# Kernel tuning notes

Measured on AMD Instinct MI355X. Metric: run time of the kernel, lower is better.

Reference implementation:

```python
import jax, jax.numpy as jnp
import numpy as np

E = 2_000_000   # edges
N = 200_000     # atoms
B = 100         # bond types (10 species, ordered pairs)
R = 13          # reduced_matrix_element (SK integrals per bond)
G = 512         # num_xgrid
T = 10          # atom types
OE = 4          # n_onsite_Es
R_MIN, R_MAX = 1.0, 6.0  # SK table distance range (Bohr-ish)


def setup_inputs() -> dict:
    key = jax.random.key(0)
    k1, k2, k3, k4, k5, k6 = jax.random.split(key, 6)
    rij = jax.random.uniform(k1, (E,), jnp.float32, 1.5, 5.5)
    edge_type = jax.random.randint(k2, (E,), 0, B, jnp.int32)
    atom_type = jax.random.randint(k3, (N,), 0, T, jnp.int32)
    xx = jnp.linspace(R_MIN, R_MAX, G, dtype=jnp.float32)  # sorted distance grid
    hopping_param = jax.random.normal(k4, (B, R, G), jnp.float32)
    overlap_param = jax.random.normal(k5, (B, R, G), jnp.float32)
    onsite_param = jax.random.normal(k6, (T, OE, 1), jnp.float32)
    return {"rij": rij, "edge_type": edge_type, "atom_type": atom_type,
            "xx": xx, "hopping_param": hopping_param,
            "overlap_param": overlap_param, "onsite_param": onsite_param}


def _interp_by_type(rij, edge_type, xx, table):
    """Fused gather + linear interpolation, keyed by edge_type.

    Replaces the original per-bond-type masked loop: for each edge, pick the
    [R, G] SK table for its bond type and linearly interpolate along the
    distance grid at rij. Returns [E, R].
    """
    g = xx.shape[0]
    # interval index for each edge (clamped -> linear extrapolation at edges)
    idx = jnp.clip(jnp.searchsorted(xx, rij, side="right") - 1, 0, g - 2)  # [E]
    x0 = xx[idx]
    x1 = xx[idx + 1]
    t = ((rij - x0) / (x1 - x0))[:, None]  # [E, 1]
    # advanced indexing on axes 0 and 2, full slice on axis 1 -> [E, R]
    y0 = table[edge_type, :, idx]
    y1 = table[edge_type, :, idx + 1]
    return y0 * (1.0 - t) + y1 * t


def reference(rij, edge_type, atom_type, xx, hopping_param, overlap_param, onsite_param):
    edge_features = _interp_by_type(rij, edge_type, xx, hopping_param)   # [E, R]
    edge_overlap = _interp_by_type(rij, edge_type, xx, overlap_param)    # [E, R]
    # dftb onsite: direct per-atom-type parameter lookup (num_paras == 1)
    node_features = onsite_param[atom_type, :, 0]                         # [N, OE]
    return edge_features, edge_overlap, node_features
```

## Files before the change

### kernel.cpp

```cpp
#include <hip/hip_runtime.h>

#define E_CNT 2000000
#define N_CNT 200000
#define B_CNT 100
#define R_CNT 13
#define G_CNT 512
#define T_CNT 10
#define OE_CNT 4

#define P_ROW 16
#define P_ONE ((size_t)B_CNT * G_CNT * P_ROW)
#define P_BYTES_TOTAL (2 * P_ONE * 4)

#define EDGES_PER_BLOCK 64
#define EDGE_BLOCKS (E_CNT / EDGES_PER_BLOCK)
#define NODE_BLOCKS ((N_CNT + 255) / 256)
#define OUT_OVL_OFF ((size_t)E_CNT * R_CNT)
#define OUT_NODE_OFF ((size_t)2 * E_CNT * R_CNT)

#define SH_STRIDE 20

__global__ __launch_bounds__(256) void repack2_kernel(
    const float* __restrict__ hopping,
    const float* __restrict__ overlap,
    float* __restrict__ Ph,
    float* __restrict__ Po)
{
    int tid = blockIdx.x * 256 + threadIdx.x;
    int g = tid & (G_CNT - 1);
    int br = tid >> 9;
    int r = br % R_CNT;
    int b = br / R_CNT;
    size_t src = (size_t)tid;
    size_t dst = ((size_t)(b * G_CNT + g)) * P_ROW + r;
    Ph[dst] = hopping[src];
    Po[dst] = overlap[src];
}

template <bool DO_NODES>
__global__ __launch_bounds__(256) void pass_kernel(
    const float* __restrict__ rij,
    const int*   __restrict__ edge_type,
    const float* __restrict__ P,
    const int*   __restrict__ atom_type,
    const float* __restrict__ onsite,
    float* __restrict__ out,
    float* __restrict__ out_nodes)
{
    if (blockIdx.x < EDGE_BLOCKS) {
        __shared__ float sh[EDGES_PER_BLOCK * SH_STRIDE];

        int tid = threadIdx.x;
        int eL = tid >> 2;
        int j  = tid & 3;
        int e  = blockIdx.x * EDGES_PER_BLOCK + eL;

        float r = rij[e];
        int b = edge_type[e];

        const float inv_dx = 511.0f / 5.0f;
        float s = (r - 1.0f) * inv_dx;
        int idx = (int)s;
        idx = max(0, min(G_CNT - 2, idx));
        float t = s - (float)idx;
        float omt = 1.0f - t;

        size_t base = ((size_t)((b << 9) + idx)) * P_ROW + 4 * j;
        float4 y0 = *(const float4*)(P + base);
        float4 y1 = *(const float4*)(P + base + P_ROW);

        float4 v;
        v.x = y0.x * omt + y1.x * t;
        v.y = y0.y * omt + y1.y * t;
        v.z = y0.z * omt + y1.z * t;
        v.w = y0.w * omt + y1.w * t;

        *(float4*)(sh + eL * SH_STRIDE + 4 * j) = v;
        __syncthreads();

        if (tid < 208) {
            unsigned f0 = (unsigned)tid * 4u;
            float4 q;
            float* qs = (float*)&q;
            #pragma unroll
            for (int k = 0; k < 4; ++k) {
                unsigned f = f0 + k;
                unsigned ee = f / 13u;
                unsigned rr = f - ee * 13u;
                qs[k] = sh[ee * SH_STRIDE + rr];
            }
            *(float4*)(out + (size_t)blockIdx.x * (EDGES_PER_BLOCK * R_CNT) + f0) = q;
        }
    } else if (DO_NODES) {
        int n = (blockIdx.x - EDGE_BLOCKS) * 256 + threadIdx.x;
        if (n < N_CNT) {
            int t = atom_type[n];
            float4 v;
            v.x = onsite[t * OE_CNT + 0];
            v.y = onsite[t * OE_CNT + 1];
            v.z = onsite[t * OE_CNT + 2];
            v.w = onsite[t * OE_CNT + 3];
            *(float4*)(out_nodes + (size_t)n * OE_CNT) = v;
        }
    }
}

__global__ __launch_bounds__(256) void dftbsk_fallback(
    const float* __restrict__ rij,
    const int*   __restrict__ edge_type,
    const int*   __restrict__ atom_type,
    const float* __restrict__ xx,
    const float* __restrict__ hopping,
    const float* __restrict__ overlap,
    const float* __restrict__ onsite,
    float*       __restrict__ out)
{
    __shared__ float sxx[G_CNT];
    for (int i = threadIdx.x; i < G_CNT; i += blockDim.x) sxx[i] = xx[i];
    __syncthreads();

    long long gid = (long long)blockIdx.x * blockDim.x + threadIdx.x;
    if (gid < E_CNT) {
        int e = (int)gid;
        float r = rij[e];
        int b = edge_type[e];
        const float inv_dx = (float)(G_CNT - 1) / 5.0f;
        int idx = (int)floorf((r - 1.0f) * inv_dx);
        idx = max(0, min(G_CNT - 2, idx));
        while (idx > 0 && r < sxx[idx]) --idx;
        while (idx < G_CNT - 2 && r >= sxx[idx + 1]) ++idx;
        float x0 = sxx[idx], x1 = sxx[idx + 1];
        float t = (r - x0) / (x1 - x0);
        float omt = 1.0f - t;
        const float* hb = hopping + (size_t)b * (R_CNT * G_CNT) + idx;
        const float* ob = overlap + (size_t)b * (R_CNT * G_CNT) + idx;
        float* outh = out + (size_t)e * R_CNT;
        float* outo = out + OUT_OVL_OFF + (size_t)e * R_CNT;
        #pragma unroll
        for (int rr = 0; rr < R_CNT; ++rr)
            outh[rr] = hb[rr * G_CNT] * omt + hb[rr * G_CNT + 1] * t;
        #pragma unroll
        for (int rr = 0; rr < R_CNT; ++rr)
            outo[rr] = ob[rr * G_CNT] * omt + ob[rr * G_CNT + 1] * t;
    } else if (gid < (long long)E_CNT + N_CNT) {
        int n = (int)(gid - E_CNT);
        int t = atom_type[n];
        float4 v;
        v.x = onsite[t * OE_CNT + 0];
        v.y = onsite[t * OE_CNT + 1];
        v.z = onsite[t * OE_CNT + 2];
        v.w = onsite[t * OE_CNT + 3];
        *(float4*)(out + OUT_NODE_OFF + (size_t)n * OE_CNT) = v;
    }
}

extern "C" void kernel_launch(void* const* d_in, const int* in_sizes, int n_in,
                              void* d_out, int out_size, void* d_ws, size_t ws_size,
                              hipStream_t stream) {
    const float* rij        = (const float*)d_in[0];
    const int*   edge_type  = (const int*)d_in[1];
    const int*   atom_type  = (const int*)d_in[2];
    const float* xx         = (const float*)d_in[3];
    const float* hopping    = (const float*)d_in[4];
    const float* overlap    = (const float*)d_in[5];
    const float* onsite     = (const float*)d_in[6];
    float* out = (float*)d_out;

    if (ws_size >= P_BYTES_TOTAL) {
        float* Ph = (float*)d_ws;
        float* Po = Ph + P_ONE;
        const int repack_total = B_CNT * R_CNT * G_CNT;
        repack2_kernel<<<repack_total / 256, 256, 0, stream>>>(hopping, overlap, Ph, Po);
        pass_kernel<true><<<EDGE_BLOCKS + NODE_BLOCKS, 256, 0, stream>>>(
            rij, edge_type, Ph, atom_type, onsite, out, out + OUT_NODE_OFF);
        pass_kernel<false><<<EDGE_BLOCKS, 256, 0, stream>>>(
            rij, edge_type, Po, atom_type, onsite, out + OUT_OVL_OFF, out + OUT_NODE_OFF);
    } else {
        const long long total = (long long)E_CNT + N_CNT;
        const int grid = (int)((total + 255) / 256);
        dftbsk_fallback<<<grid, 256, 0, stream>>>(rij, edge_type, atom_type, xx,
                                                  hopping, overlap, onsite, out);
    }
}
```

Before: 279.0 us.

## Fuse hopping and overlap passes with interleaved table layout and nontemporal IO

Repacks the hopping and overlap tables into one interleaved 128-byte row per (bond type, grid point), so that a single fused kernel interpolates both outputs from adjacent cache lines. This removes the second pass, which re-read rij and edge_type and launched a second large grid. Output and input streams also switch to nontemporal loads and stores, to keep them from displacing the gathered table in cache. In exchange the table footprint doubles per row and each block uses twice the shared memory.

```diff
diff --git a/kernel.cpp b/kernel.cpp
--- a/kernel.cpp
+++ b/kernel.cpp
@@ -8,9 +8,9 @@
 #define T_CNT 10
 #define OE_CNT 4
 
-#define P_ROW 16
-#define P_ONE ((size_t)B_CNT * G_CNT * P_ROW)
-#define P_BYTES_TOTAL (2 * P_ONE * 4)
+#define P2_ROW 32
+#define P2_FLOATS ((size_t)B_CNT * G_CNT * P2_ROW)
+#define P2_BYTES (P2_FLOATS * 4)
 
 #define EDGES_PER_BLOCK 64
 #define EDGE_BLOCKS (E_CNT / EDGES_PER_BLOCK)
@@ -20,43 +20,54 @@
 
 #define SH_STRIDE 20
 
-__global__ __launch_bounds__(256) void repack2_kernel(
+typedef float v4f __attribute__((ext_vector_type(4)));
+
+__global__ __launch_bounds__(256) void repack_interleave_kernel(
     const float* __restrict__ hopping,
     const float* __restrict__ overlap,
-    float* __restrict__ Ph,
-    float* __restrict__ Po)
+    float* __restrict__ P2)
 {
     int tid = blockIdx.x * 256 + threadIdx.x;
+    int b = tid >> 9;
     int g = tid & (G_CNT - 1);
-    int br = tid >> 9;
-    int r = br % R_CNT;
-    int b = br / R_CNT;
-    size_t src = (size_t)tid;
-    size_t dst = ((size_t)(b * G_CNT + g)) * P_ROW + r;
-    Ph[dst] = hopping[src];
-    Po[dst] = overlap[src];
+    float h[16], o[16];
+    #pragma unroll
+    for (int r = 0; r < R_CNT; ++r) {
+        size_t src = (((size_t)b * R_CNT + r) << 9) + g;
+        h[r] = hopping[src];
+        o[r] = overlap[src];
+    }
+    h[13] = h[14] = h[15] = 0.0f;
+    o[13] = o[14] = o[15] = 0.0f;
+    float* dst = P2 + (size_t)tid * P2_ROW;
+    #pragma unroll
+    for (int q = 0; q < 4; ++q) {
+        v4f hv = { h[4*q], h[4*q+1], h[4*q+2], h[4*q+3] };
+        v4f ov = { o[4*q], o[4*q+1], o[4*q+2], o[4*q+3] };
+        *(v4f*)(dst + 4 * q)      = hv;
+        *(v4f*)(dst + 16 + 4 * q) = ov;
+    }
 }
 
-template <bool DO_NODES>
-__global__ __launch_bounds__(256) void pass_kernel(
+__global__ __launch_bounds__(256) void fused_kernel(
     const float* __restrict__ rij,
     const int*   __restrict__ edge_type,
-    const float* __restrict__ P,
+    const float* __restrict__ P2,
     const int*   __restrict__ atom_type,
     const float* __restrict__ onsite,
-    float* __restrict__ out,
-    float* __restrict__ out_nodes)
+    float* __restrict__ out)
 {
     if (blockIdx.x < EDGE_BLOCKS) {
-        __shared__ float sh[EDGES_PER_BLOCK * SH_STRIDE];
+        __shared__ float shh[EDGES_PER_BLOCK * SH_STRIDE];
+        __shared__ float sho[EDGES_PER_BLOCK * SH_STRIDE];
 
         int tid = threadIdx.x;
         int eL = tid >> 2;
         int j  = tid & 3;
         int e  = blockIdx.x * EDGES_PER_BLOCK + eL;
 
-        float r = rij[e];
-        int b = edge_type[e];
+        float r = __builtin_nontemporal_load(rij + e);
+        int   b = __builtin_nontemporal_load(edge_type + e);
 
         const float inv_dx = 511.0f / 5.0f;
         float s = (r - 1.0f) * inv_dx;
@@ -65,42 +76,45 @@
         float t = s - (float)idx;
         float omt = 1.0f - t;
 
-        size_t base = ((size_t)((b << 9) + idx)) * P_ROW + 4 * j;
-        float4 y0 = *(const float4*)(P + base);
-        float4 y1 = *(const float4*)(P + base + P_ROW);
+        const float* row = P2 + ((size_t)((b << 9) + idx)) * P2_ROW + 4 * j;
+        v4f h0 = *(const v4f*)(row);
+        v4f h1 = *(const v4f*)(row + P2_ROW);
+        v4f o0 = *(const v4f*)(row + 16);
+        v4f o1 = *(const v4f*)(row + 16 + P2_ROW);
 
-        float4 v;
-        v.x = y0.x * omt + y1.x * t;
-        v.y = y0.y * omt + y1.y * t;
-        v.z = y0.z * omt + y1.z * t;
-        v.w = y0.w * omt + y1.w * t;
+        v4f vh = h0 * omt + h1 * t;
+        v4f vo = o0 * omt + o1 * t;
 
-        *(float4*)(sh + eL * SH_STRIDE + 4 * j) = v;
+        *(v4f*)(shh + eL * SH_STRIDE + 4 * j) = vh;
+        *(v4f*)(sho + eL * SH_STRIDE + 4 * j) = vo;
         __syncthreads();
 
         if (tid < 208) {
             unsigned f0 = (unsigned)tid * 4u;
-            float4 q;
-            float* qs = (float*)&q;
+            float ph[4], po[4];
             #pragma unroll
             for (int k = 0; k < 4; ++k) {
                 unsigned f = f0 + k;
                 unsigned ee = f / 13u;
                 unsigned rr = f - ee * 13u;
-                qs[k] = sh[ee * SH_STRIDE + rr];
+                ph[k] = shh[ee * SH_STRIDE + rr];
+                po[k] = sho[ee * SH_STRIDE + rr];
             }
-            *(float4*)(out + (size_t)blockIdx.x * (EDGES_PER_BLOCK * R_CNT) + f0) = q;
+            v4f qh = { ph[0], ph[1], ph[2], ph[3] };
+            v4f qo = { po[0], po[1], po[2], po[3] };
+            size_t ob = (size_t)blockIdx.x * (EDGES_PER_BLOCK * R_CNT) + f0;
+            __builtin_nontemporal_store(qh, (v4f*)(out + ob));
+            __builtin_nontemporal_store(qo, (v4f*)(out + OUT_OVL_OFF + ob));
         }
-    } else if (DO_NODES) {
+    } else {
         int n = (blockIdx.x - EDGE_BLOCKS) * 256 + threadIdx.x;
         if (n < N_CNT) {
             int t = atom_type[n];
-            float4 v;
-            v.x = onsite[t * OE_CNT + 0];
-            v.y = onsite[t * OE_CNT + 1];
-            v.z = onsite[t * OE_CNT + 2];
-            v.w = onsite[t * OE_CNT + 3];
-            *(float4*)(out_nodes + (size_t)n * OE_CNT) = v;
+            v4f v = { onsite[t * OE_CNT + 0],
+                      onsite[t * OE_CNT + 1],
+                      onsite[t * OE_CNT + 2],
+                      onsite[t * OE_CNT + 3] };
+            __builtin_nontemporal_store(v, (v4f*)(out + OUT_NODE_OFF + (size_t)n * OE_CNT));
         }
     }
 }
@@ -166,15 +180,12 @@
     const float* onsite     = (const float*)d_in[6];
     float* out = (float*)d_out;
 
-    if (ws_size >= P_BYTES_TOTAL) {
-        float* Ph = (float*)d_ws;
-        float* Po = Ph + P_ONE;
-        const int repack_total = B_CNT * R_CNT * G_CNT;
-        repack2_kernel<<<repack_total / 256, 256, 0, stream>>>(hopping, overlap, Ph, Po);
-        pass_kernel<true><<<EDGE_BLOCKS + NODE_BLOCKS, 256, 0, stream>>>(
-            rij, edge_type, Ph, atom_type, onsite, out, out + OUT_NODE_OFF);
-        pass_kernel<false><<<EDGE_BLOCKS, 256, 0, stream>>>(
-            rij, edge_type, Po, atom_type, onsite, out + OUT_OVL_OFF, out + OUT_NODE_OFF);
+    if (ws_size >= P2_BYTES) {
+        float* P2 = (float*)d_ws;
+        repack_interleave_kernel<<<(B_CNT * G_CNT) / 256, 256, 0, stream>>>(
+            hopping, overlap, P2);
+        fused_kernel<<<EDGE_BLOCKS + NODE_BLOCKS, 256, 0, stream>>>(
+            rij, edge_type, P2, atom_type, onsite, out);
     } else {
         const long long total = (long long)E_CNT + N_CNT;
         const int grid = (int)((total + 255) / 256);
```

New measurement: 265.9 us. -4.7%, faster.
